# Performance work log

Measured on AMD Instinct MI355X. Metric: run time of the kernel, lower is better.

Reference implementation:

```python
import jax, jax.numpy as jnp
import numpy as np

EPS = 1e-6

def _l2normalize(x, axis=1):
    # matches torch: x / sqrt(sum(x^2) + eps)
    norm = jnp.sqrt(jnp.sum(x * x, axis=axis, keepdims=True) + EPS)
    return x / norm


def setup_inputs() -> dict:
    key = jax.random.key(0)
    k1, k2, k3 = jax.random.split(key, 3)
    B, C, H, W = 8, 64, 48, 48
    x = jax.random.normal(k1, (B, C, H, W), dtype=jnp.float32)
    v = jax.random.normal(k2, (B, C, H, W), dtype=jnp.float32)
    pos = jax.random.normal(k3, (B, C, H, W), dtype=jnp.float32)
    # learned scalar parameters (init values from the torch module)
    gamma = jnp.float32(0.0)
    beta_gamma = jnp.float32(10.0)
    sum_gamma0 = jnp.float32(0.0)
    sum_gamma1 = jnp.float32(0.0)
    return {"x": x, "v": v, "pos": pos, "gamma": gamma,
            "beta_gamma": beta_gamma, "sum_gamma0": sum_gamma0,
            "sum_gamma1": sum_gamma1}


def reference(x, v, pos, gamma, beta_gamma, sum_gamma0, sum_gamma1):
    B, C, H, W = x.shape
    N = H * W
    # q and k are computed identically in the original module; compute once.
    q = _l2normalize(x + gamma * pos, axis=1)          # [B, C, H, W]
    qf = q.reshape(B, C, N)                             # [B, C, N]
    vf = v.reshape(B, v.shape[1], N)                    # [B, Cv, N]
    # scores[b, n, m] = <q[:, n], k[:, m]>; learned temperature beta_gamma
    scores = jnp.einsum('bcn,bcm->bnm', qf, qf) * beta_gamma  # [B, N, N]
    beta = jax.nn.softmax(scores, axis=-1)              # [B, N, N]
    # o = v @ beta^T  => o[b, c, n] = sum_m v[b, c, m] * beta[b, n, m]
    o = jnp.einsum('bcm,bnm->bcn', vf, beta).reshape(B, vf.shape[1], H, W)
    e0 = jnp.exp(sum_gamma0)
    e1 = jnp.exp(sum_gamma1)
    tot = e0 + e1
    out = (e0 / tot) * o + (e1 / tot) * v
    return out, beta.reshape(B, N, H, W)
```

## Files before the change

kernel.cpp:

```cpp
#include <hip/hip_runtime.h>
#include <hip/hip_bf16.h>

#define B_  8
#define C_  64
#define N_  2304
#define TS  64
#define NT_ (N_ / TS)
#define LDP 72
#define SPL 4
#define MTS (NT_ / SPL)

typedef __attribute__((ext_vector_type(8))) short  short8;
typedef __attribute__((ext_vector_type(4))) float  floatx4;

struct Hdr { int f32mode; float gamma, bg, cmax, w0, w1; };

__device__ __forceinline__ float bf2f(unsigned short u) {
  return __uint_as_float(((unsigned int)u) << 16);
}
__device__ __forceinline__ unsigned short f2bf(float f) {
  unsigned int x = __float_as_uint(f);
  x += 0x7fff + ((x >> 16) & 1);
  return (unsigned short)(x >> 16);
}

__global__ void detect_k(const void* g, const void* bgp, const void* s0,
                         const void* s1, Hdr* h) {
  if (threadIdx.x == 0 && blockIdx.x == 0) {
    int f32 = (((const unsigned short*)bgp)[0] == 0) ? 1 : 0;
    float gamma, bg, sg0, sg1;
    if (f32) {
      gamma = ((const float*)g)[0];  bg  = ((const float*)bgp)[0];
      sg0   = ((const float*)s0)[0]; sg1 = ((const float*)s1)[0];
    } else {
      gamma = bf2f(((const unsigned short*)g)[0]);
      bg    = bf2f(((const unsigned short*)bgp)[0]);
      sg0   = bf2f(((const unsigned short*)s0)[0]);
      sg1   = bf2f(((const unsigned short*)s1)[0]);
    }
    float e0 = __expf(sg0), e1 = __expf(sg1);
    h->f32mode = f32;
    h->gamma = gamma;
    h->bg = bg;
    h->cmax = fabsf(bg);
    h->w0 = e0 / (e0 + e1);
    h->w1 = e1 / (e0 + e1);
  }
}

__global__ __launch_bounds__(64)
void prep_q(const void* __restrict__ xv, const void* __restrict__ posv,
            const Hdr* __restrict__ h, unsigned short* __restrict__ qT) {
  int t = blockIdx.x * 64 + threadIdx.x;
  int b = t / N_;
  int n = t - b * N_;
  const bool f32 = h->f32mode;
  float gamma = h->gamma;
  float vals[C_];
  float s = 0.f;
  if (f32) {
    const float* xp = (const float*)xv  + (size_t)b * C_ * N_ + n;
    const float* pp = (const float*)posv + (size_t)b * C_ * N_ + n;
#pragma unroll
    for (int c = 0; c < C_; ++c) {
      float val = xp[(size_t)c * N_] + gamma * pp[(size_t)c * N_];
      vals[c] = val;  s += val * val;
    }
  } else {
    const unsigned short* xp = (const unsigned short*)xv  + (size_t)b * C_ * N_ + n;
    const unsigned short* pp = (const unsigned short*)posv + (size_t)b * C_ * N_ + n;
#pragma unroll
    for (int c = 0; c < C_; ++c) {
      float val = bf2f(xp[(size_t)c * N_]) + gamma * bf2f(pp[(size_t)c * N_]);
      vals[c] = val;  s += val * val;
    }
  }
  float inv = rsqrtf(s + 1e-6f);
  unsigned int* qrow = reinterpret_cast<unsigned int*>(qT + (size_t)t * C_);
#pragma unroll
  for (int c = 0; c < C_; c += 2) {
    qrow[c >> 1] = (unsigned int)f2bf(vals[c] * inv)
                 | ((unsigned int)f2bf(vals[c + 1] * inv) << 16);
  }
}

__global__ __launch_bounds__(256)
void pass1_rowsum(const unsigned short* __restrict__ qT,
                  const void* __restrict__ vraw,
                  const Hdr* __restrict__ h,
                  unsigned short* __restrict__ vb,
                  float* __restrict__ rowsum_part) {
  __shared__ unsigned short qm[TS * LDP];
  int bx  = blockIdx.x;
  int tid = threadIdx.x;
  {
    int t = bx * 256 + tid;
    unsigned int* vb32 = reinterpret_cast<unsigned int*>(vb);
    if (h->f32mode) {
      const float* vf = (const float*)vraw;
#pragma unroll
      for (int k = 0; k < 2; ++k) {
        int i = t + k * 294912;
        float f0 = vf[2 * i], f1 = vf[2 * i + 1];
        vb32[i] = (unsigned int)f2bf(f0) | ((unsigned int)f2bf(f1) << 16);
      }
    } else {
      const unsigned int* v32 = (const unsigned int*)vraw;
#pragma unroll
      for (int k = 0; k < 2; ++k) {
        int i = t + k * 294912;
        vb32[i] = v32[i];
      }
    }
  }
  int s  = bx & (SPL - 1);
  int nt = (bx >> 2) % NT_;
  int b  = bx / (SPL * NT_);
  int n0 = nt * TS;
  int wave = tid >> 6;
  int lane = tid & 63;
  int quad = lane >> 4;
  int l15  = lane & 15;
  float bg = h->bg, cmax = h->cmax;
  const unsigned short* abase =
      qT + ((size_t)(b * N_ + n0 + 16 * wave + l15)) * C_ + quad * 8;
  short8 a0 = *reinterpret_cast<const short8*>(abase);
  short8 a1 = *reinterpret_cast<const short8*>(abase + 32);
  float acc[4] = {0.f, 0.f, 0.f, 0.f};
  int mt0 = s * MTS;
  for (int mt = mt0; mt < mt0 + MTS; ++mt) {
    int m0 = mt * TS;
    __syncthreads();
#pragma unroll
    for (int k = 0; k < 2; ++k) {
      int chunk = tid + 256 * k;
      int row = chunk >> 3;
      int col = (chunk & 7) * 8;
      short8 vv = *reinterpret_cast<const short8*>(
          qT + ((size_t)(b * N_ + m0 + row)) * C_ + col);
      *reinterpret_cast<short8*>(&qm[row * LDP + col]) = vv;
    }
    __syncthreads();
#pragma unroll
    for (int j = 0; j < 4; ++j) {
      short8 b0 = *reinterpret_cast<const short8*>(&qm[(j * 16 + l15) * LDP + quad * 8]);
      short8 b1 = *reinterpret_cast<const short8*>(&qm[(j * 16 + l15) * LDP + 32 + quad * 8]);
      floatx4 d = {0.f, 0.f, 0.f, 0.f};
      d = __builtin_amdgcn_mfma_f32_16x16x32_bf16(a0, b0, d, 0, 0, 0);
      d = __builtin_amdgcn_mfma_f32_16x16x32_bf16(a1, b1, d, 0, 0, 0);
#pragma unroll
      for (int r = 0; r < 4; ++r)
        acc[r] += __expf(d[r] * bg - cmax);
    }
  }
#pragma unroll
  for (int r = 0; r < 4; ++r) {
    float vv = acc[r];
    vv += __shfl_xor(vv, 1);
    vv += __shfl_xor(vv, 2);
    vv += __shfl_xor(vv, 4);
    vv += __shfl_xor(vv, 8);
    acc[r] = vv;
  }
  if (l15 == 0) {
#pragma unroll
    for (int r = 0; r < 4; ++r)
      rowsum_part[((size_t)(b * N_ + n0 + 16 * wave + quad * 4 + r)) * SPL + s]
          = acc[r];
  }
}

__global__ __launch_bounds__(256)
void pass2_attn(const unsigned short* __restrict__ qT,
                const unsigned short* __restrict__ vb,
                const Hdr* __restrict__ h,
                const float* __restrict__ rowsum_part,
                float* __restrict__ opart,
                void* __restrict__ dout) {
  __shared__ unsigned short qm[TS * LDP];
  __shared__ unsigned short vt[TS * LDP];
  __shared__ unsigned short pt[TS * LDP];
  int bx = blockIdx.x;
  int s  = bx & (SPL - 1);
  int nt = (bx >> 2) % NT_;
  int b  = bx / (SPL * NT_);
  int n0 = nt * TS;
  int tid  = threadIdx.x;
  int wave = tid >> 6;
  int lane = tid & 63;
  int quad = lane >> 4;
  int l15  = lane & 15;
  const bool f32 = h->f32mode;
  float bg = h->bg, cmax = h->cmax;
  unsigned short* out16  = (unsigned short*)dout;
  unsigned short* beta16 = out16 + (size_t)B_ * C_ * N_;
  float* beta32 = (float*)dout + (size_t)B_ * C_ * N_;

  const unsigned short* abase =
      qT + ((size_t)(b * N_ + n0 + 16 * wave + l15)) * C_ + quad * 8;
  short8 a0 = *reinterpret_cast<const short8*>(abase);
  short8 a1 = *reinterpret_cast<const short8*>(abase + 32);
  float inv[4];
#pragma unroll
  for (int r = 0; r < 4; ++r) {
    floatx4 rs = *reinterpret_cast<const floatx4*>(
        rowsum_part + ((size_t)(b * N_ + n0 + 16 * wave + quad * 4 + r)) * SPL);
    inv[r] = 1.f / (rs[0] + rs[1] + rs[2] + rs[3]);
  }
  floatx4 oacc[4] = {{0.f,0.f,0.f,0.f},{0.f,0.f,0.f,0.f},
                     {0.f,0.f,0.f,0.f},{0.f,0.f,0.f,0.f}};
  int mtb = s * MTS;
  for (int mt = mtb; mt < mtb + MTS; ++mt) {
    int m0 = mt * TS;
    __syncthreads();
#pragma unroll
    for (int k = 0; k < 2; ++k) {
      int chunk = tid + 256 * k;
      int row = chunk >> 3;
      int col = (chunk & 7) * 8;
      short8 qv = *reinterpret_cast<const short8*>(
          qT + ((size_t)(b * N_ + m0 + row)) * C_ + col);
      *reinterpret_cast<short8*>(&qm[row * LDP + col]) = qv;
      short8 vv = *reinterpret_cast<const short8*>(
          vb + ((size_t)(b * C_ + row)) * N_ + m0 + col);
      *reinterpret_cast<short8*>(&vt[row * LDP + col]) = vv;
    }
    __syncthreads();
#pragma unroll
    for (int j = 0; j < 4; ++j) {
      short8 b0 = *reinterpret_cast<const short8*>(&qm[(j * 16 + l15) * LDP + quad * 8]);
      short8 b1 = *reinterpret_cast<const short8*>(&qm[(j * 16 + l15) * LDP + 32 + quad * 8]);
      floatx4 d = {0.f, 0.f, 0.f, 0.f};
      d = __builtin_amdgcn_mfma_f32_16x16x32_bf16(a0, b0, d, 0, 0, 0);
      d = __builtin_amdgcn_mfma_f32_16x16x32_bf16(a1, b1, d, 0, 0, 0);
#pragma unroll
      for (int r = 0; r < 4; ++r) {
        float p = __expf(d[r] * bg - cmax) * inv[r];
        pt[(16 * wave + quad * 4 + r) * LDP + j * 16 + l15] = f2bf(p);
        if (f32) {
          beta32[((size_t)(b * N_ + n0 + 16 * wave + quad * 4 + r)) * N_
                 + m0 + j * 16 + l15] = p;
        }
      }
    }
    __syncthreads();
    if (!f32) {
#pragma unroll
      for (int k = 0; k < 2; ++k) {
        int chunk = tid + 256 * k;
        int row = chunk >> 3;
        int col = (chunk & 7) * 8;
        short8 pv = *reinterpret_cast<const short8*>(&pt[row * LDP + col]);
        *reinterpret_cast<short8*>(
            beta16 + ((size_t)(b * N_ + n0 + row)) * N_ + m0 + col) = pv;
      }
    }
    short8 av0 = *reinterpret_cast<const short8*>(&vt[(16 * wave + l15) * LDP + quad * 8]);
    short8 av1 = *reinterpret_cast<const short8*>(&vt[(16 * wave + l15) * LDP + 32 + quad * 8]);
#pragma unroll
    for (int j = 0; j < 4; ++j) {
      short8 bp0 = *reinterpret_cast<const short8*>(&pt[(j * 16 + l15) * LDP + quad * 8]);
      short8 bp1 = *reinterpret_cast<const short8*>(&pt[(j * 16 + l15) * LDP + 32 + quad * 8]);
      oacc[j] = __builtin_amdgcn_mfma_f32_16x16x32_bf16(av0, bp0, oacc[j], 0, 0, 0);
      oacc[j] = __builtin_amdgcn_mfma_f32_16x16x32_bf16(av1, bp1, oacc[j], 0, 0, 0);
    }
  }
  float* op = opart + (size_t)s * (B_ * C_ * N_);
#pragma unroll
  for (int j = 0; j < 4; ++j) {
#pragma unroll
    for (int r = 0; r < 4; ++r) {
      int c = 16 * wave + quad * 4 + r;
      int n = n0 + 16 * j + l15;
      op[((size_t)(b * C_ + c)) * N_ + n] = oacc[j][r];
    }
  }
}

__global__ __launch_bounds__(256)
void blend_k(const float* __restrict__ opart, const void* __restrict__ vraw,
             const Hdr* __restrict__ h, void* __restrict__ dout) {
  int t = blockIdx.x * 256 + threadIdx.x;
  const int STR = (B_ * C_ * N_) / 4;
  const floatx4* p = reinterpret_cast<const floatx4*>(opart);
  floatx4 o  = p[t];
  floatx4 o1 = p[t + STR];
  floatx4 o2 = p[t + 2 * STR];
  floatx4 o3 = p[t + 3 * STR];
#pragma unroll
  for (int k = 0; k < 4; ++k) o[k] = (o[k] + o1[k]) + (o2[k] + o3[k]);
  float w0 = h->w0, w1 = h->w1;
  if (h->f32mode) {
    floatx4 vv = reinterpret_cast<const floatx4*>(vraw)[t];
    floatx4 r;
#pragma unroll
    for (int k = 0; k < 4; ++k) r[k] = w0 * o[k] + w1 * vv[k];
    reinterpret_cast<floatx4*>(dout)[t] = r;
  } else {
    unsigned long long v64 =
        reinterpret_cast<const unsigned long long*>(vraw)[t];
    unsigned long long rr = 0;
#pragma unroll
    for (int k = 0; k < 4; ++k) {
      float vf = bf2f((unsigned short)(v64 >> (16 * k)));
      rr |= ((unsigned long long)f2bf(w0 * o[k] + w1 * vf)) << (16 * k);
    }
    reinterpret_cast<unsigned long long*>(dout)[t] = rr;
  }
}

extern "C" void kernel_launch(void* const* d_in, const int* in_sizes, int n_in,
                              void* d_out, int out_size, void* d_ws, size_t ws_size,
                              hipStream_t stream) {
  const void* x     = d_in[0];
  const void* v     = d_in[1];
  const void* pos   = d_in[2];
  const void* gamma = d_in[3];
  const void* bg    = d_in[4];
  const void* sg0   = d_in[5];
  const void* sg1   = d_in[6];

  char* ws = (char*)d_ws;
  Hdr* hdr = (Hdr*)ws;
  unsigned short* qT = (unsigned short*)(ws + 256);
  unsigned short* vb = qT + (size_t)B_ * N_ * C_;
  float* rowsum_part = (float*)(ws + 256 + (size_t)B_ * N_ * C_ * 4);
  float* opart = rowsum_part + (size_t)B_ * N_ * SPL;

  detect_k<<<dim3(1), dim3(64), 0, stream>>>(gamma, bg, sg0, sg1, hdr);
  prep_q<<<dim3((B_ * N_) / 64), dim3(64), 0, stream>>>(x, pos, hdr, qT);
  pass1_rowsum<<<dim3(B_ * NT_ * SPL), dim3(256), 0, stream>>>(qT, v, hdr, vb, rowsum_part);
  pass2_attn<<<dim3(B_ * NT_ * SPL), dim3(256), 0, stream>>>(qT, vb, hdr, rowsum_part, opart, d_out);
  blend_k<<<dim3((B_ * C_ * N_) / 1024), dim3(256), 0, stream>>>(opart, v, hdr, d_out);
}
```

Measured before the change: 225.1 us.

## Load MFMA operands directly from global and double-buffer P tile with one barrier

```diff
diff --git a/kernel.cpp b/kernel.cpp
--- a/kernel.cpp
+++ b/kernel.cpp
@@ -90,7 +90,6 @@
                   const Hdr* __restrict__ h,
                   unsigned short* __restrict__ vb,
                   float* __restrict__ rowsum_part) {
-  __shared__ unsigned short qm[TS * LDP];
   int bx  = blockIdx.x;
   int tid = threadIdx.x;
   {
@@ -130,21 +129,12 @@
   int mt0 = s * MTS;
   for (int mt = mt0; mt < mt0 + MTS; ++mt) {
     int m0 = mt * TS;
-    __syncthreads();
-#pragma unroll
-    for (int k = 0; k < 2; ++k) {
-      int chunk = tid + 256 * k;
-      int row = chunk >> 3;
-      int col = (chunk & 7) * 8;
-      short8 vv = *reinterpret_cast<const short8*>(
-          qT + ((size_t)(b * N_ + m0 + row)) * C_ + col);
-      *reinterpret_cast<short8*>(&qm[row * LDP + col]) = vv;
-    }
-    __syncthreads();
 #pragma unroll
     for (int j = 0; j < 4; ++j) {
-      short8 b0 = *reinterpret_cast<const short8*>(&qm[(j * 16 + l15) * LDP + quad * 8]);
-      short8 b1 = *reinterpret_cast<const short8*>(&qm[(j * 16 + l15) * LDP + 32 + quad * 8]);
+      const unsigned short* qb =
+          qT + ((size_t)(b * N_ + m0 + j * 16 + l15)) * C_ + quad * 8;
+      short8 b0 = *reinterpret_cast<const short8*>(qb);
+      short8 b1 = *reinterpret_cast<const short8*>(qb + 32);
       floatx4 d = {0.f, 0.f, 0.f, 0.f};
       d = __builtin_amdgcn_mfma_f32_16x16x32_bf16(a0, b0, d, 0, 0, 0);
       d = __builtin_amdgcn_mfma_f32_16x16x32_bf16(a1, b1, d, 0, 0, 0);
@@ -177,9 +167,7 @@
                 const float* __restrict__ rowsum_part,
                 float* __restrict__ opart,
                 void* __restrict__ dout) {
-  __shared__ unsigned short qm[TS * LDP];
-  __shared__ unsigned short vt[TS * LDP];
-  __shared__ unsigned short pt[TS * LDP];
+  __shared__ unsigned short pt[2][TS * LDP];
   int bx = blockIdx.x;
   int s  = bx & (SPL - 1);
   int nt = (bx >> 2) % NT_;
@@ -210,57 +198,49 @@
   floatx4 oacc[4] = {{0.f,0.f,0.f,0.f},{0.f,0.f,0.f,0.f},
                      {0.f,0.f,0.f,0.f},{0.f,0.f,0.f,0.f}};
   int mtb = s * MTS;
-  for (int mt = mtb; mt < mtb + MTS; ++mt) {
-    int m0 = mt * TS;
-    __syncthreads();
-#pragma unroll
-    for (int k = 0; k < 2; ++k) {
-      int chunk = tid + 256 * k;
-      int row = chunk >> 3;
-      int col = (chunk & 7) * 8;
-      short8 qv = *reinterpret_cast<const short8*>(
-          qT + ((size_t)(b * N_ + m0 + row)) * C_ + col);
-      *reinterpret_cast<short8*>(&qm[row * LDP + col]) = qv;
-      short8 vv = *reinterpret_cast<const short8*>(
-          vb + ((size_t)(b * C_ + row)) * N_ + m0 + col);
-      *reinterpret_cast<short8*>(&vt[row * LDP + col]) = vv;
-    }
-    __syncthreads();
+  const unsigned short* vrow = vb + ((size_t)(b * C_ + 16 * wave + l15)) * N_;
+  for (int it = 0; it < MTS; ++it) {
+    int m0 = (mtb + it) * TS;
+    unsigned short* ptc = pt[it & 1];
+    short8 av0 = *reinterpret_cast<const short8*>(vrow + m0 + quad * 8);
+    short8 av1 = *reinterpret_cast<const short8*>(vrow + m0 + 32 + quad * 8);
 #pragma unroll
     for (int j = 0; j < 4; ++j) {
-      short8 b0 = *reinterpret_cast<const short8*>(&qm[(j * 16 + l15) * LDP + quad * 8]);
-      short8 b1 = *reinterpret_cast<const short8*>(&qm[(j * 16 + l15) * LDP + 32 + quad * 8]);
+      const unsigned short* qb =
+          qT + ((size_t)(b * N_ + m0 + j * 16 + l15)) * C_ + quad * 8;
+      short8 b0 = *reinterpret_cast<const short8*>(qb);
+      short8 b1 = *reinterpret_cast<const short8*>(qb + 32);
       floatx4 d = {0.f, 0.f, 0.f, 0.f};
       d = __builtin_amdgcn_mfma_f32_16x16x32_bf16(a0, b0, d, 0, 0, 0);
       d = __builtin_amdgcn_mfma_f32_16x16x32_bf16(a1, b1, d, 0, 0, 0);
 #pragma unroll
       for (int r = 0; r < 4; ++r) {
         float p = __expf(d[r] * bg - cmax) * inv[r];
-        pt[(16 * wave + quad * 4 + r) * LDP + j * 16 + l15] = f2bf(p);
+        ptc[(16 * wave + quad * 4 + r) * LDP + j * 16 + l15] = f2bf(p);
         if (f32) {
           beta32[((size_t)(b * N_ + n0 + 16 * wave + quad * 4 + r)) * N_
                  + m0 + j * 16 + l15] = p;
         }
       }
     }
-    __syncthreads();
+    asm volatile("s_waitcnt lgkmcnt(0)" ::: "memory");
+    __builtin_amdgcn_s_barrier();
+    __builtin_amdgcn_sched_barrier(0);
     if (!f32) {
 #pragma unroll
       for (int k = 0; k < 2; ++k) {
         int chunk = tid + 256 * k;
         int row = chunk >> 3;
         int col = (chunk & 7) * 8;
-        short8 pv = *reinterpret_cast<const short8*>(&pt[row * LDP + col]);
+        short8 pv = *reinterpret_cast<const short8*>(&ptc[row * LDP + col]);
         *reinterpret_cast<short8*>(
             beta16 + ((size_t)(b * N_ + n0 + row)) * N_ + m0 + col) = pv;
       }
     }
-    short8 av0 = *reinterpret_cast<const short8*>(&vt[(16 * wave + l15) * LDP + quad * 8]);
-    short8 av1 = *reinterpret_cast<const short8*>(&vt[(16 * wave + l15) * LDP + 32 + quad * 8]);
 #pragma unroll
     for (int j = 0; j < 4; ++j) {
-      short8 bp0 = *reinterpret_cast<const short8*>(&pt[(j * 16 + l15) * LDP + quad * 8]);
-      short8 bp1 = *reinterpret_cast<const short8*>(&pt[(j * 16 + l15) * LDP + 32 + quad * 8]);
+      short8 bp0 = *reinterpret_cast<const short8*>(&ptc[(j * 16 + l15) * LDP + quad * 8]);
+      short8 bp1 = *reinterpret_cast<const short8*>(&ptc[(j * 16 + l15) * LDP + 32 + quad * 8]);
       oacc[j] = __builtin_amdgcn_mfma_f32_16x16x32_bf16(av0, bp0, oacc[j], 0, 0, 0);
       oacc[j] = __builtin_amdgcn_mfma_f32_16x16x32_bf16(av1, bp1, oacc[j], 0, 0, 0);
     }
```

Result: slower. 276.8 us (+23.0%).
